# Kernel tuning notes

Measured on AMD Instinct MI355X. Metric: run time of the kernel, lower is better.

## Reference

```python
import jax, jax.numpy as jnp
import numpy as np

D_MODEL, H, D_K, D_V, D_FF = 1024, 16, 64, 64, 4096
B, L = 2, 2048
EPS = 1e-5


def layer_norm(x, g, b):
    mu = jnp.mean(x, axis=-1, keepdims=True)
    var = jnp.mean(jnp.square(x - mu), axis=-1, keepdims=True)
    return (x - mu) * jax.lax.rsqrt(var + EPS) * g + b


def setup_inputs() -> dict:
    key = jax.random.key(0)
    ks = jax.random.split(key, 12)
    s = 0.02
    x = jax.random.normal(ks[0], (B, L, D_MODEL), dtype=jnp.float32)
    Wq = jax.random.normal(ks[1], (H, D_MODEL, D_K), dtype=jnp.float32) * s
    Wk = jax.random.normal(ks[2], (H, D_MODEL, D_K), dtype=jnp.float32) * s
    Wv = jax.random.normal(ks[3], (H, D_MODEL, D_V), dtype=jnp.float32) * s
    bq = jnp.zeros((H, D_K), dtype=jnp.float32)
    bk = jnp.zeros((H, D_K), dtype=jnp.float32)
    bv = jnp.zeros((H, D_V), dtype=jnp.float32)
    Wo = jax.random.normal(ks[4], (H * D_V, D_MODEL), dtype=jnp.float32) * s
    W1 = jax.random.normal(ks[5], (D_MODEL, D_FF), dtype=jnp.float32) * s
    b1 = jnp.zeros((D_FF,), dtype=jnp.float32)
    W2 = jax.random.normal(ks[6], (D_FF, D_MODEL), dtype=jnp.float32) * s
    ln1_g = jnp.ones((D_MODEL,), dtype=jnp.float32)
    ln1_b = jnp.zeros((D_MODEL,), dtype=jnp.float32)
    ln2_g = jnp.ones((D_MODEL,), dtype=jnp.float32)
    ln2_b = jnp.zeros((D_MODEL,), dtype=jnp.float32)
    return dict(x=x, Wq=Wq, bq=bq, Wk=Wk, bk=bk, Wv=Wv, bv=bv, Wo=Wo,
                ln1_g=ln1_g, ln1_b=ln1_b, W1=W1, b1=b1, W2=W2,
                ln2_g=ln2_g, ln2_b=ln2_b)


def reference(x, Wq, bq, Wk, bk, Wv, bv, Wo, ln1_g, ln1_b, W1, b1, W2, ln2_g, ln2_b):
    # Batched multi-head attention (all heads at once, equivalent to the
    # per-head Python loop in the original module).
    Q = jnp.einsum('bld,hdk->bhlk', x, Wq) + bq[None, :, None, :]
    K = jnp.einsum('bld,hdk->bhlk', x, Wk) + bk[None, :, None, :]
    V = jnp.einsum('bld,hdv->bhlv', x, Wv) + bv[None, :, None, :]
    scores = jnp.einsum('bhlk,bhmk->bhlm', Q, K) * (1.0 / jnp.sqrt(jnp.float32(D_K)))
    attn = jax.nn.softmax(scores, axis=-1)
    O = jnp.einsum('bhlm,bhmv->bhlv', attn, V)        # [b,h,l,dv]
    O = jnp.transpose(O, (0, 2, 1, 3)).reshape(x.shape[0], x.shape[1], H * D_V)
    mha = O @ Wo                                       # [b,l,d_model]
    # residual + LayerNorm (dropout_prob=0 -> identity)
    h1 = layer_norm(x + mha, ln1_g, ln1_b)
    ff = jax.nn.relu(h1 @ W1 + b1) @ W2
    return layer_norm(h1 + ff, ln2_g, ln2_b)
```

## Files before the change

kernel.cpp:

```cpp
#include <hip/hip_runtime.h>

typedef unsigned short u16;
typedef unsigned int u32;
typedef short bf16x8 __attribute__((ext_vector_type(8)));
typedef float f32x4 __attribute__((ext_vector_type(4)));
typedef unsigned int u32x2 __attribute__((ext_vector_type(2)));
typedef unsigned int u32x4 __attribute__((ext_vector_type(4)));

#define D_MODEL 1024
#define NH 16
#define DK 64
#define DFF 4096
#define BATCH 2
#define SEQ 2048
#define BL (BATCH*SEQ)
#define NQKV 3072
#define Q_SCALE 0.18033688011f

__device__ __forceinline__ float bfraw2f(u16 u) {
    union { u32 i; float f; } c; c.i = ((u32)u) << 16; return c.f;
}
__device__ __forceinline__ u16 f2bfraw(float f) {
    union { float f; u32 i; } c; c.f = f;
    u32 i = c.i;
    u32 lsb = (i >> 16) & 1u;
    i += 0x7fffu + lsb;
    return (u16)(i >> 16);
}
__device__ __forceinline__ u32 fasu(float f) {
    union { float f; u32 i; } c; c.f = f; return c.i;
}
__device__ __forceinline__ u32 pack_bf2(float lo, float hi) {
    return __builtin_amdgcn_perm(fasu(hi) + 0x8000u, fasu(lo) + 0x8000u,
                                 0x07060302u);
}
__device__ __forceinline__ void gload_lds16(const u16* g, u16* l) {
    __builtin_amdgcn_global_load_lds(
        (const __attribute__((address_space(1))) void*)g,
        (__attribute__((address_space(3))) void*)l, 16, 0, 0);
}

__global__ __launch_bounds__(256) void cast_f32_bf16(const float* __restrict__ in,
                                                     u16* __restrict__ out) {
    int i = (blockIdx.x * 256 + threadIdx.x) * 4;
    f32x4 v = *(const f32x4*)&in[i];
#pragma unroll
    for (int j = 0; j < 4; j++) out[i + j] = f2bfraw(v[j]);
}


__global__ __launch_bounds__(256) void transpose2d(const float* __restrict__ in,
                                                   u16* __restrict__ out,
                                                   int R, int C) {
    __shared__ u16 t[64][65];
    int c0 = blockIdx.x * 64, r0 = blockIdx.y * 64;
    int col = threadIdx.x & 63, rr = threadIdx.x >> 6;
    for (int i = rr; i < 64; i += 4)
        t[i][col] = f2bfraw(in[(size_t)(r0 + i) * C + c0 + col]);
    __syncthreads();
    for (int i = rr; i < 64; i += 4)
        out[(size_t)(c0 + i) * R + r0 + col] = t[col][i];
}

__global__ __launch_bounds__(256) void transpose_wqkv(const float* __restrict__ Wq,
                                                      const float* __restrict__ Wk,
                                                      const float* __restrict__ Wv,
                                                      u16* __restrict__ out) {
    __shared__ u16 t[64][65];
    int d0 = blockIdx.x * 64;
    int h = blockIdx.y;
    int ms = blockIdx.z;
    const float* W = (ms == 0) ? Wq : (ms == 1) ? Wk : Wv;
    const float* src = W + (size_t)h * D_MODEL * DK;
    int col = threadIdx.x & 63, rr = threadIdx.x >> 6;
    for (int i = rr; i < 64; i += 4)
        t[i][col] = f2bfraw(src[(size_t)(d0 + i) * DK + col]);
    __syncthreads();
    u16* dst = out + (size_t)(ms * 1024 + h * 64) * D_MODEL;
    for (int i = rr; i < 64; i += 4)
        dst[(size_t)i * D_MODEL + d0 + col] = t[col][i];
}

__global__ __launch_bounds__(256) void concat_bias(const float* __restrict__ bq,
                                                   const float* __restrict__ bk,
                                                   const float* __restrict__ bv,
                                                   float* __restrict__ out) {
    int i = blockIdx.x * 256 + threadIdx.x;
    out[i] = (i < 1024) ? bq[i] : (i < 2048) ? bk[i - 1024] : bv[i - 2048];
}


template <int BM, int OUT_F32, int RELU, int HASBIAS, int SPLITK, int SCALEQ, int VSTORE>
__global__ __launch_bounds__(512, 2) void gemm2(const u16* __restrict__ A,
                                                const u16* __restrict__ Bt,
                                                const float* __restrict__ bias,
                                                void* __restrict__ Cout,
                                                u16* __restrict__ vtout,
                                                int M, int N, int K) {
    constexpr int MF = BM / 32;
    __shared__ __attribute__((aligned(16))) u16 As[2][BM * 64];
    __shared__ __attribute__((aligned(16))) u16 Bs[2][256 * 64];
    const int tid = threadIdx.x;
    const int lane = tid & 63, wid = tid >> 6;
    const int quad = lane >> 4, l16 = lane & 15;

    int nwg = gridDim.x * gridDim.y;
    int flat = blockIdx.y * gridDim.x + blockIdx.x;
    if ((nwg & 7) == 0) {
        int q = nwg >> 3;
        flat = (flat & 7) * q + (flat >> 3);
    }
    const int m0 = (flat % gridDim.x) * BM;
    const int n0 = (flat / gridDim.x) * 256;

    const int z = (SPLITK > 1) ? blockIdx.z : 0;
    const int Klen = K / SPLITK;
    const int NT = Klen / 64;
    const int kb0 = z * Klen;

    const int wrow = (wid >> 2) * (BM / 2);
    const int wcol = (wid & 3) * 64;

    f32x4 acc[MF][4];
#pragma unroll
    for (int i = 0; i < MF; i++)
#pragma unroll
        for (int j = 0; j < 4; j++) acc[i][j] = (f32x4){0.f, 0.f, 0.f, 0.f};

    auto stage = [&](int kb, int slot) {
#pragma unroll
        for (int p = 0; p < BM / 64; p++) {
            int ew = p * 512 + wid * 64;
            int e = ew + lane;
            int row = e >> 3, ch = e & 7;
            gload_lds16(&A[(size_t)(m0 + row) * K + kb + ((ch ^ (row & 7)) * 8)],
                        &As[slot][ew * 8]);
        }
#pragma unroll
        for (int p = 0; p < 4; p++) {
            int ew = p * 512 + wid * 64;
            int e = ew + lane;
            int row = e >> 3, ch = e & 7;
            gload_lds16(&Bt[(size_t)(n0 + row) * K + kb + ((ch ^ (row & 7)) * 8)],
                        &Bs[slot][ew * 8]);
        }
    };

    stage(kb0, 0);
    for (int t = 0; t < NT; t++) {
        __syncthreads();
        if (t + 1 < NT) stage(kb0 + (t + 1) * 64, (t + 1) & 1);
        const u16* as = As[t & 1];
        const u16* bs = Bs[t & 1];
        __builtin_amdgcn_s_setprio(1);
        bf16x8 bfr[4][2];
#pragma unroll
        for (int j = 0; j < 4; j++) {
            int rb = wcol + j * 16 + l16;
#pragma unroll
            for (int kh = 0; kh < 2; kh++)
                bfr[j][kh] = *(const bf16x8*)&bs[rb * 64 + (((kh * 4 + quad) ^ (rb & 7)) * 8)];
        }
#pragma unroll
        for (int i = 0; i < MF; i++) {
            int ra = wrow + i * 16 + l16;
            bf16x8 a0 = *(const bf16x8*)&as[ra * 64 + ((quad ^ (ra & 7)) * 8)];
            bf16x8 a1 = *(const bf16x8*)&as[ra * 64 + (((4 + quad) ^ (ra & 7)) * 8)];
#pragma unroll
            for (int j = 0; j < 4; j++) {
                acc[i][j] = __builtin_amdgcn_mfma_f32_16x16x32_bf16(a0, bfr[j][0], acc[i][j], 0, 0, 0);
                acc[i][j] = __builtin_amdgcn_mfma_f32_16x16x32_bf16(a1, bfr[j][1], acc[i][j], 0, 0, 0);
            }
        }
        __builtin_amdgcn_s_setprio(0);
    }

    if (VSTORE && n0 >= 2048) {
#pragma unroll
        for (int i = 0; i < MF; i++) {
            int row0 = m0 + wrow + i * 16 + quad * 4;
            int bb = row0 >> 11, l = row0 & 2047;
#pragma unroll
            for (int j = 0; j < 4; j++) {
                int col = n0 + wcol + j * 16 + l16;
                float bv = HASBIAS ? bias[col] : 0.f;
                int dv = col - 2048;
                u32x2 w;
                w.x = pack_bf2(acc[i][j][0] + bv, acc[i][j][1] + bv);
                w.y = pack_bf2(acc[i][j][2] + bv, acc[i][j][3] + bv);
                *(u32x2*)&vtout[((size_t)(bb * 1024 + dv)) * 2048 + l] = w;
            }
        }
        return;
    }

    float* outf = (float*)Cout + (size_t)z * M * N;
#pragma unroll
    for (int i = 0; i < MF; i++) {
#pragma unroll
        for (int j = 0; j < 4; j++) {
#pragma unroll
            for (int r = 0; r < 4; r++) {
                int row = m0 + wrow + i * 16 + quad * 4 + r;
                int col = n0 + wcol + j * 16 + l16;
                float v = acc[i][j][r];
                if (HASBIAS) v += bias[col];
                if (RELU) v = v > 0.f ? v : 0.f;
                if (SCALEQ && col < 1024) v *= Q_SCALE;
                if (OUT_F32)
                    outf[(size_t)row * N + col] = v;
                else
                    ((u16*)Cout)[(size_t)row * N + col] = f2bfraw(v);
            }
        }
    }
}

__global__ __launch_bounds__(512, 4) void attn_kernel(const u16* __restrict__ qkv,
                                                      const u16* __restrict__ vt,
                                                      u16* __restrict__ O) {
    __shared__ __attribute__((aligned(16))) u16 Ks[2][128 * 64];
    __shared__ __attribute__((aligned(16))) u16 Vs[64 * 128];

    const int tid = threadIdx.x;
    const int lane = tid & 63, wid = tid >> 6;
    const int quad = lane >> 4, l16 = lane & 15;
    const int sw = l16 & 7;
    const int b = blockIdx.z, h = blockIdx.y;
    const int q0 = blockIdx.x * 128 + wid * 16;

    const size_t qrow = (size_t)(b * SEQ + q0 + l16) * NQKV + h * DK;
    const bf16x8 qf0 = *(const bf16x8*)&qkv[qrow + quad * 8];
    const bf16x8 qf1 = *(const bf16x8*)&qkv[qrow + 32 + quad * 8];

    const u16* Kbase = qkv + (size_t)(b * SEQ) * NQKV + D_MODEL + h * DK;
    const u16* Vbase = vt + (size_t)((b * NH + h) * DK) * SEQ;

    f32x4 oacc[4];
#pragma unroll
    for (int d = 0; d < 4; d++) oacc[d] = (f32x4){0.f, 0.f, 0.f, 0.f};
    float lr = 0.f;
    const f32x4 Z = {0.f, 0.f, 0.f, 0.f};

    auto stage_k = [&](int kt2, int buf) {
#pragma unroll
        for (int p = 0; p < 2; p++) {
            int seg = p * 8 + wid;
            int row = seg * 8 + (lane >> 3);
            int chunk = (lane & 7) ^ (lane >> 3);
            gload_lds16(&Kbase[(size_t)(kt2 + row) * NQKV + chunk * 8],
                        &Ks[buf][seg * 512]);
        }
    };
    bf16x8 vreg[2];
    auto load_v = [&](int kt2) {
#pragma unroll
        for (int p = 0; p < 2; p++) {
            int s = p * 512 + tid;
            vreg[p] = *(const bf16x8*)&Vbase[(size_t)(s >> 4) * SEQ + kt2 + (s & 15) * 8];
        }
    };
    stage_k(0, 0);
    load_v(0);

    for (int t = 0; t < SEQ / 128; t++) {
        const int kt = t * 128;
#pragma unroll
        for (int p = 0; p < 2; p++) {
            int s = p * 512 + tid;
            int vr = s >> 4, vc = s & 15;
            int chunkA = (vc >> 2) * 4 + (vc & 1) * 2;
            int rem = ((vc >> 1) & 1) * 4;
            u32x4 kv = __builtin_bit_cast(u32x4, vreg[p]);
            *(u32x2*)&Vs[vr * 128 + ((chunkA ^ (vr & 7)) * 8) + rem] =
                (u32x2){kv.x, kv.y};
            *(u32x2*)&Vs[vr * 128 + (((chunkA + 1) ^ (vr & 7)) * 8) + rem] =
                (u32x2){kv.z, kv.w};
        }
        __syncthreads();

        if (t + 1 < SEQ / 128) {
            stage_k(kt + 128, (t + 1) & 1);
            load_v(kt + 128);
        }

        const u16* kb = Ks[t & 1];

        f32x4 sacc[8];
        __builtin_amdgcn_s_setprio(1);
#pragma unroll
        for (int nt = 0; nt < 8; nt++) {
            const u16* krow = &kb[(nt * 16 + l16) * 64];
            bf16x8 kf0 = *(const bf16x8*)&krow[(quad ^ sw) * 8];
            bf16x8 kf1 = *(const bf16x8*)&krow[((4 + quad) ^ sw) * 8];
            f32x4 s0 = __builtin_amdgcn_mfma_f32_16x16x32_bf16(kf0, qf0, Z, 0, 0, 0);
            sacc[nt] = __builtin_amdgcn_mfma_f32_16x16x32_bf16(kf1, qf1, s0, 0, 0, 0);
        }
        __builtin_amdgcn_s_setprio(0);

        u32 wreg[8][2];
#pragma unroll
        for (int nt = 0; nt < 8; nt++) {
            float p0 = __builtin_amdgcn_exp2f(sacc[nt][0]);
            float p1 = __builtin_amdgcn_exp2f(sacc[nt][1]);
            float p2 = __builtin_amdgcn_exp2f(sacc[nt][2]);
            float p3 = __builtin_amdgcn_exp2f(sacc[nt][3]);
            lr += (p0 + p1) + (p2 + p3);
            wreg[nt][0] = pack_bf2(p0, p1);
            wreg[nt][1] = pack_bf2(p2, p3);
        }

        __builtin_amdgcn_s_setprio(1);
#pragma unroll
        for (int ks = 0; ks < 4; ks++) {
            u32x4 pw = (u32x4){wreg[2 * ks][0], wreg[2 * ks][1],
                               wreg[2 * ks + 1][0], wreg[2 * ks + 1][1]};
            bf16x8 pf = __builtin_bit_cast(bf16x8, pw);
#pragma unroll
            for (int d = 0; d < 4; d++) {
                bf16x8 vf = *(const bf16x8*)&Vs[(d * 16 + l16) * 128 +
                                                (((ks * 4 + quad) ^ sw) * 8)];
                oacc[d] = __builtin_amdgcn_mfma_f32_16x16x32_bf16(vf, pf, oacc[d], 0, 0, 0);
            }
        }
        __builtin_amdgcn_s_setprio(0);
        __syncthreads();
    }

    lr += __shfl_xor(lr, 16, 64);
    lr += __shfl_xor(lr, 32, 64);
    float iv = 1.f / lr;

    size_t row = (size_t)(b * SEQ + q0 + l16);
#pragma unroll
    for (int d = 0; d < 4; d++) {
        float o0 = oacc[d][0] * iv, o1 = oacc[d][1] * iv;
        float o2 = oacc[d][2] * iv, o3 = oacc[d][3] * iv;
        u32x2 w;
        w.x = ((u32)f2bfraw(o1) << 16) | f2bfraw(o0);
        w.y = ((u32)f2bfraw(o3) << 16) | f2bfraw(o2);
        *(u32x2*)&O[row * D_MODEL + h * DK + d * 16 + quad * 4] = w;
    }
}

__global__ __launch_bounds__(256) void ln3_kernel(const float* __restrict__ xa,
                                                  const float* __restrict__ xb,
                                                  const float* __restrict__ xc,
                                                  const float* __restrict__ g,
                                                  const float* __restrict__ be,
                                                  u16* __restrict__ out_bf,
                                                  float* __restrict__ out_f) {
    int row = blockIdx.x;
    int tid = threadIdx.x;
    const float* pa = xa + (size_t)row * D_MODEL;
    const float* pb = xb + (size_t)row * D_MODEL;
    const float* pc = xc + (size_t)row * D_MODEL;
    int c = tid * 4;
    f32x4 av = *(const f32x4*)&pa[c];
    f32x4 bv = *(const f32x4*)&pb[c];
    f32x4 cv = *(const f32x4*)&pc[c];
    float v[4];
    float s = 0.f, ss = 0.f;
#pragma unroll
    for (int i = 0; i < 4; i++) {
        v[i] = av[i] + bv[i] + cv[i];
        s += v[i];
        ss += v[i] * v[i];
    }
#pragma unroll
    for (int off = 32; off; off >>= 1) {
        s += __shfl_down(s, off, 64);
        ss += __shfl_down(ss, off, 64);
    }
    __shared__ float red[8];
    int wid = tid >> 6, lane = tid & 63;
    if (lane == 0) { red[wid] = s; red[4 + wid] = ss; }
    __syncthreads();
    if (tid == 0) {
        red[0] = red[0] + red[1] + red[2] + red[3];
        red[4] = red[4] + red[5] + red[6] + red[7];
    }
    __syncthreads();
    float mu = red[0] * (1.f / D_MODEL);
    float var = red[4] * (1.f / D_MODEL) - mu * mu;
    float rs = rsqrtf(var + 1e-5f);
#pragma unroll
    for (int i = 0; i < 4; i++) {
        float o = (v[i] - mu) * rs * g[c + i] + be[c + i];
        if (out_f) out_f[(size_t)row * D_MODEL + c + i] = o;
        if (out_bf) out_bf[(size_t)row * D_MODEL + c + i] = f2bfraw(o);
    }
}

extern "C" void kernel_launch(void* const* d_in, const int* in_sizes, int n_in,
                              void* d_out, int out_size, void* d_ws, size_t ws_size,
                              hipStream_t stream) {
    const float* x   = (const float*)d_in[0];
    const float* Wq  = (const float*)d_in[1];
    const float* bq  = (const float*)d_in[2];
    const float* Wk  = (const float*)d_in[3];
    const float* bk  = (const float*)d_in[4];
    const float* Wv  = (const float*)d_in[5];
    const float* bv  = (const float*)d_in[6];
    const float* Wo  = (const float*)d_in[7];
    const float* g1  = (const float*)d_in[8];
    const float* be1 = (const float*)d_in[9];
    const float* W1  = (const float*)d_in[10];
    const float* b1  = (const float*)d_in[11];
    const float* W2  = (const float*)d_in[12];
    const float* g2  = (const float*)d_in[13];
    const float* be2 = (const float*)d_in[14];

    char* w = (char*)d_ws;
    auto alloc = [&](size_t bytes) {
        char* p = w;
        w += (bytes + 255) & ~(size_t)255;
        return p;
    };
    u16* wqkv_t = (u16*)alloc((size_t)NQKV * D_MODEL * 2);
    u16* wo_t   = (u16*)alloc((size_t)D_MODEL * D_MODEL * 2);
    u16* w1_t   = (u16*)alloc((size_t)DFF * D_MODEL * 2);
    u16* w2_t   = (u16*)alloc((size_t)D_MODEL * DFF * 2);
    float* bqkv = (float*)alloc((size_t)NQKV * 4);
    u16* x_bf   = (u16*)alloc((size_t)BL * D_MODEL * 2);
    u16* qkvbuf = (u16*)alloc((size_t)BL * NQKV * 2);
    u16* vtbuf  = (u16*)alloc((size_t)BATCH * NH * DK * SEQ * 2);
    u16* obuf   = (u16*)alloc((size_t)BL * D_MODEL * 2);
    float* mha_p = (float*)alloc((size_t)2 * BL * D_MODEL * 4);
    u16* h1_bf  = (u16*)alloc((size_t)BL * D_MODEL * 2);
    float* h1_f = (float*)alloc((size_t)BL * D_MODEL * 4);
    u16* ffa    = (u16*)alloc((size_t)BL * DFF * 2);
    float* ffb_p = (float*)alloc((size_t)2 * BL * D_MODEL * 4);

    cast_f32_bf16<<<dim3(BL * D_MODEL / 1024), 256, 0, stream>>>(x, x_bf);
    transpose_wqkv<<<dim3(16, 16, 3), 256, 0, stream>>>(Wq, Wk, Wv, wqkv_t);
    transpose2d<<<dim3(16, 16), 256, 0, stream>>>(Wo, wo_t, 1024, 1024);
    transpose2d<<<dim3(64, 16), 256, 0, stream>>>(W1, w1_t, 1024, 4096);
    transpose2d<<<dim3(16, 64), 256, 0, stream>>>(W2, w2_t, 4096, 1024);
    concat_bias<<<dim3(12), 256, 0, stream>>>(bq, bk, bv, bqkv);

    gemm2<256, 0, 0, 1, 1, 1, 1><<<dim3(16, 12), 512, 0, stream>>>(
        x_bf, wqkv_t, bqkv, qkvbuf, vtbuf, BL, NQKV, D_MODEL);
    attn_kernel<<<dim3(16, 16, 2), 512, 0, stream>>>(qkvbuf, vtbuf, obuf);
    gemm2<128, 1, 0, 0, 2, 0, 0><<<dim3(32, 4, 2), 512, 0, stream>>>(
        obuf, wo_t, nullptr, mha_p, nullptr, BL, D_MODEL, D_MODEL);
    ln3_kernel<<<dim3(BL), 256, 0, stream>>>(x, mha_p, mha_p + (size_t)BL * D_MODEL,
                                             g1, be1, h1_bf, h1_f);
    gemm2<256, 0, 1, 1, 1, 0, 0><<<dim3(16, 16), 512, 0, stream>>>(
        h1_bf, w1_t, b1, ffa, nullptr, BL, DFF, D_MODEL);
    gemm2<128, 1, 0, 0, 2, 0, 0><<<dim3(32, 4, 2), 512, 0, stream>>>(
        ffa, w2_t, nullptr, ffb_p, nullptr, BL, D_MODEL, DFF);
    ln3_kernel<<<dim3(BL), 256, 0, stream>>>(h1_f, ffb_p, ffb_p + (size_t)BL * D_MODEL,
                                             g2, be2, nullptr, (float*)d_out);
}
```

Baseline: 376.9 us.

## Prefetch GEMM tiles two stages ahead and retile split-K GEMMs to 128x128

The GEMM kernel now preloads the first two K-tiles. Each iteration waits with an explicit vmcnt and a barrier, then issues the load for tile t+2 into the buffer it just consumed. This lets global-to-LDS loads overlap more fully with the MFMA work. The kernel is also generalized over BN and thread count. The out-projection and FF2 GEMMs switch to 128x128 tiles with 256 threads, doubling the workgroup count to improve occupancy and load balance. The hand-set vmcnt(8) only works because every tile configuration issues exactly 8 loads per thread per stage, and the extra barrier per iteration adds sync cost.

```diff
diff --git a/kernel.cpp b/kernel.cpp
--- a/kernel.cpp
+++ b/kernel.cpp
@@ -90,16 +90,20 @@
 }
 
 
-template <int BM, int OUT_F32, int RELU, int HASBIAS, int SPLITK, int SCALEQ, int VSTORE>
-__global__ __launch_bounds__(512, 2) void gemm2(const u16* __restrict__ A,
-                                                const u16* __restrict__ Bt,
-                                                const float* __restrict__ bias,
-                                                void* __restrict__ Cout,
-                                                u16* __restrict__ vtout,
-                                                int M, int N, int K) {
-    constexpr int MF = BM / 32;
+template <int BM, int BN, int T, int OUT_F32, int RELU, int HASBIAS, int SPLITK,
+          int SCALEQ, int VSTORE>
+__global__ __launch_bounds__(T, 2) void gemm3(const u16* __restrict__ A,
+                                              const u16* __restrict__ Bt,
+                                              const float* __restrict__ bias,
+                                              void* __restrict__ Cout,
+                                              u16* __restrict__ vtout,
+                                              int M, int N, int K) {
+    constexpr int WGN = BN / 64;
+    constexpr int WGM = (T / 64) / WGN;
+    constexpr int PWM = BM / WGM;
+    constexpr int MF = PWM / 16;
     __shared__ __attribute__((aligned(16))) u16 As[2][BM * 64];
-    __shared__ __attribute__((aligned(16))) u16 Bs[2][256 * 64];
+    __shared__ __attribute__((aligned(16))) u16 Bs[2][BN * 64];
     const int tid = threadIdx.x;
     const int lane = tid & 63, wid = tid >> 6;
     const int quad = lane >> 4, l16 = lane & 15;
@@ -111,15 +115,15 @@
         flat = (flat & 7) * q + (flat >> 3);
     }
     const int m0 = (flat % gridDim.x) * BM;
-    const int n0 = (flat / gridDim.x) * 256;
+    const int n0 = (flat / gridDim.x) * BN;
 
     const int z = (SPLITK > 1) ? blockIdx.z : 0;
     const int Klen = K / SPLITK;
     const int NT = Klen / 64;
     const int kb0 = z * Klen;
 
-    const int wrow = (wid >> 2) * (BM / 2);
-    const int wcol = (wid & 3) * 64;
+    const int wrow = (wid / WGN) * PWM;
+    const int wcol = (wid % WGN) * 64;
 
     f32x4 acc[MF][4];
 #pragma unroll
@@ -129,16 +133,16 @@
 
     auto stage = [&](int kb, int slot) {
 #pragma unroll
-        for (int p = 0; p < BM / 64; p++) {
-            int ew = p * 512 + wid * 64;
+        for (int p = 0; p < (BM * 8) / T; p++) {
+            int ew = p * T + wid * 64;
             int e = ew + lane;
             int row = e >> 3, ch = e & 7;
             gload_lds16(&A[(size_t)(m0 + row) * K + kb + ((ch ^ (row & 7)) * 8)],
                         &As[slot][ew * 8]);
         }
 #pragma unroll
-        for (int p = 0; p < 4; p++) {
-            int ew = p * 512 + wid * 64;
+        for (int p = 0; p < (BN * 8) / T; p++) {
+            int ew = p * T + wid * 64;
             int e = ew + lane;
             int row = e >> 3, ch = e & 7;
             gload_lds16(&Bt[(size_t)(n0 + row) * K + kb + ((ch ^ (row & 7)) * 8)],
@@ -147,9 +151,17 @@
     };
 
     stage(kb0, 0);
+    if (NT > 1) stage(kb0 + 64, 1);
+
     for (int t = 0; t < NT; t++) {
-        __syncthreads();
-        if (t + 1 < NT) stage(kb0 + (t + 1) * 64, (t + 1) & 1);
+        if (t + 1 < NT) {
+            asm volatile("s_waitcnt vmcnt(8)" ::: "memory");
+        } else {
+            asm volatile("s_waitcnt vmcnt(0)" ::: "memory");
+        }
+        __builtin_amdgcn_s_barrier();
+        __builtin_amdgcn_sched_barrier(0);
+
         const u16* as = As[t & 1];
         const u16* bs = Bs[t & 1];
         __builtin_amdgcn_s_setprio(1);
@@ -173,6 +185,10 @@
             }
         }
         __builtin_amdgcn_s_setprio(0);
+        __builtin_amdgcn_sched_barrier(0);
+        __builtin_amdgcn_s_barrier();
+        __builtin_amdgcn_sched_barrier(0);
+        if (t + 2 < NT) stage(kb0 + (t + 2) * 64, t & 1);
     }
 
     if (VSTORE && n0 >= 2048) {
@@ -439,16 +455,16 @@
     transpose2d<<<dim3(16, 64), 256, 0, stream>>>(W2, w2_t, 4096, 1024);
     concat_bias<<<dim3(12), 256, 0, stream>>>(bq, bk, bv, bqkv);
 
-    gemm2<256, 0, 0, 1, 1, 1, 1><<<dim3(16, 12), 512, 0, stream>>>(
+    gemm3<256, 256, 512, 0, 0, 1, 1, 1, 1><<<dim3(16, 12), 512, 0, stream>>>(
         x_bf, wqkv_t, bqkv, qkvbuf, vtbuf, BL, NQKV, D_MODEL);
     attn_kernel<<<dim3(16, 16, 2), 512, 0, stream>>>(qkvbuf, vtbuf, obuf);
-    gemm2<128, 1, 0, 0, 2, 0, 0><<<dim3(32, 4, 2), 512, 0, stream>>>(
+    gemm3<128, 128, 256, 1, 0, 0, 2, 0, 0><<<dim3(32, 8, 2), 256, 0, stream>>>(
         obuf, wo_t, nullptr, mha_p, nullptr, BL, D_MODEL, D_MODEL);
     ln3_kernel<<<dim3(BL), 256, 0, stream>>>(x, mha_p, mha_p + (size_t)BL * D_MODEL,
                                              g1, be1, h1_bf, h1_f);
-    gemm2<256, 0, 1, 1, 1, 0, 0><<<dim3(16, 16), 512, 0, stream>>>(
+    gemm3<256, 256, 512, 0, 1, 1, 1, 0, 0><<<dim3(16, 16), 512, 0, stream>>>(
         h1_bf, w1_t, b1, ffa, nullptr, BL, DFF, D_MODEL);
-    gemm2<128, 1, 0, 0, 2, 0, 0><<<dim3(32, 4, 2), 512, 0, stream>>>(
+    gemm3<128, 128, 256, 1, 0, 0, 2, 0, 0><<<dim3(32, 8, 2), 256, 0, stream>>>(
         ffa, w2_t, nullptr, ffb_p, nullptr, BL, D_MODEL, DFF);
     ln3_kernel<<<dim3(BL), 256, 0, stream>>>(h1_f, ffb_p, ffb_p + (size_t)BL * D_MODEL,
                                              g2, be2, nullptr, (float*)d_out);
```

Measured after the change: 369.7 us. About the same (-1.9%).
